# Performance work log

Measured on AMD Instinct MI355X. Metric: run time of the kernel, lower is better.

Reference implementation:

```python
import jax, jax.numpy as jnp
import numpy as np

EPS = 1e-12

def setup_inputs() -> dict:
    key = jax.random.key(0)
    k1, k2 = jax.random.split(key)
    B, C, H, W = 16, 256, 64, 64
    x1 = jax.random.normal(k1, (B, C, H, W), dtype=jnp.float32)
    x2 = jax.random.normal(k2, (B, C, H, W), dtype=jnp.float32)
    return {"x1": x1, "x2": x2}

def _l2norm(x):
    # F.normalize(p=2, dim=2, eps=1e-12): divide by max(norm, eps)
    n = jnp.linalg.norm(x, axis=2, keepdims=True)
    return x / jnp.maximum(n, EPS)

def reference(x1, x2):
    B, C, H, W = x1.shape
    x111 = x1.reshape(B, C, H * W)            # [B,C,N]
    x211 = x2.reshape(B, C, H * W)
    x11 = _l2norm(x111)
    x21 = _l2norm(x211)
    # four CxC score matmuls, fused pairwise adds
    attn1 = jnp.einsum('bcn,bdn->bcd', x11, x11)
    attn2 = jnp.einsum('bcn,bdn->bcd', x21, x21)
    attn0 = jnp.einsum('bcn,bdn->bcd', x21, x11)
    attn00 = jnp.einsum('bcn,bdn->bcd', x11, x21)
    attn11 = jax.nn.softmax(attn1 + attn0, axis=-1)   # [B,C,C]
    attn22 = jax.nn.softmax(attn2 + attn00, axis=-1)
    # back-projection, torch transpose(1,2).reshape(B,C,H,W) semantics
    y1 = jnp.einsum('bcd,bdn->bcn', attn11, x111)     # [B,C,N]
    y2 = jnp.einsum('bcd,bdn->bcn', attn22, x211)
    x1_o = jnp.swapaxes(y1, 1, 2).reshape(B, C, H, W) + x1
    x2_o = jnp.swapaxes(y2, 1, 2).reshape(B, C, H, W) + x2
    return x1_o + x2_o
```

## Files before the change

### kernel.cpp

```cpp
#include <hip/hip_runtime.h>
#include <hip/hip_bf16.h>

#define B_ 16
#define C_ 256
#define N_ 4096
#define CN_ (C_ * N_)

typedef __attribute__((ext_vector_type(8))) short bf16x8_t;
typedef __attribute__((ext_vector_type(4))) float f32x4_t;
typedef unsigned int u32;
typedef unsigned short u16;

__device__ __forceinline__ u16 f2bf(float f) {
    __hip_bfloat16 h = __float2bfloat16(f);
    return __builtin_bit_cast(u16, h);
}
__device__ __forceinline__ float bf2f(u16 u) {
    return __builtin_bit_cast(float, (u32)u << 16);
}

__device__ __forceinline__ void gl_lds16(const void* g, void* l) {
    __builtin_amdgcn_global_load_lds(
        (const __attribute__((address_space(1))) u32*)(g),
        (__attribute__((address_space(3))) u32*)(l), 16, 0, 0);
}

__global__ __launch_bounds__(256) void knorm(const float* __restrict__ x1,
                                             const float* __restrict__ x2,
                                             u16* __restrict__ x1n,
                                             u16* __restrict__ x2n,
                                             u16* __restrict__ sN,
                                             u16* __restrict__ sxb,
                                             float* __restrict__ norms) {
    int row = blockIdx.x;
    int t = threadIdx.x;
    const float4* r1 = (const float4*)(x1 + (size_t)row * N_);
    const float4* r2 = (const float4*)(x2 + (size_t)row * N_);
    float4 a[4], b[4];
    float s1 = 0.f, s2 = 0.f;
#pragma unroll
    for (int p = 0; p < 4; ++p) {
        a[p] = r1[p * 256 + t];
        b[p] = r2[p * 256 + t];
        s1 += a[p].x * a[p].x + a[p].y * a[p].y + a[p].z * a[p].z + a[p].w * a[p].w;
        s2 += b[p].x * b[p].x + b[p].y * b[p].y + b[p].z * b[p].z + b[p].w * b[p].w;
    }
#pragma unroll
    for (int m = 32; m; m >>= 1) { s1 += __shfl_xor(s1, m); s2 += __shfl_xor(s2, m); }
    __shared__ float red[2][4];
    int wid = t >> 6;
    if ((t & 63) == 0) { red[0][wid] = s1; red[1][wid] = s2; }
    __syncthreads();
    s1 = red[0][0] + red[0][1] + red[0][2] + red[0][3];
    s2 = red[1][0] + red[1][1] + red[1][2] + red[1][3];
    float n1 = fmaxf(sqrtf(s1), 1e-12f);
    float n2 = fmaxf(sqrtf(s2), 1e-12f);
    if (t == 0) {
        int bb = row >> 8, cc = row & 255;
        norms[(bb * 2 + 0) * 256 + cc] = n1;
        norms[(bb * 2 + 1) * 256 + cc] = n2;
    }
    float i1 = 1.0f / n1, i2 = 1.0f / n2;
    u16* o1 = x1n + (size_t)row * N_;
    u16* o2 = x2n + (size_t)row * N_;
    u16* os = sN + (size_t)row * N_;
    u16* or_ = sxb + (size_t)row * N_;
#pragma unroll
    for (int p = 0; p < 4; ++p) {
        ushort4 w1, w2, ws, wr;
        w1.x = f2bf(a[p].x * i1); w1.y = f2bf(a[p].y * i1);
        w1.z = f2bf(a[p].z * i1); w1.w = f2bf(a[p].w * i1);
        w2.x = f2bf(b[p].x * i2); w2.y = f2bf(b[p].y * i2);
        w2.z = f2bf(b[p].z * i2); w2.w = f2bf(b[p].w * i2);
        ws.x = f2bf(a[p].x * i1 + b[p].x * i2); ws.y = f2bf(a[p].y * i1 + b[p].y * i2);
        ws.z = f2bf(a[p].z * i1 + b[p].z * i2); ws.w = f2bf(a[p].w * i1 + b[p].w * i2);
        wr.x = f2bf(a[p].x + b[p].x); wr.y = f2bf(a[p].y + b[p].y);
        wr.z = f2bf(a[p].z + b[p].z); wr.w = f2bf(a[p].w + b[p].w);
        size_t off = (size_t)(p * 256 + t) * 4;
        *(ushort4*)(o1 + off) = w1;
        *(ushort4*)(o2 + off) = w2;
        *(ushort4*)(os + off) = ws;
        *(ushort4*)(or_ + off) = wr;
    }
}

__global__ __launch_bounds__(256) void klogits(const u16* __restrict__ sN,
                                               const u16* __restrict__ x1n,
                                               const u16* __restrict__ x2n,
                                               float* __restrict__ logits) {
    int bid = blockIdx.x;
    int xcd = bid & 7;
    int u = bid >> 3;
    int b = xcd + 8 * (u & 1);
    int tile = u >> 1;
    int c0 = (tile & 3) * 64;
    int d0 = (tile >> 2) * 64;

    __shared__ u16 lds[3 * 4096];

    int t = threadIdx.x, lane = t & 63, wid = t >> 6;
    int w = wid & 1, chalf = wid >> 1;

    const char* tb[3];
    tb[0] = (const char*)(sN  + (size_t)b * CN_ + (size_t)c0 * N_);
    tb[1] = (const char*)(x1n + (size_t)b * CN_ + (size_t)d0 * N_);
    tb[2] = (const char*)(x2n + (size_t)b * CN_ + (size_t)d0 * N_);
    const char* gsrc[6];
    char* ldst[6];
#pragma unroll
    for (int qq = 0; qq < 6; ++qq) {
        int q = wid * 6 + qq;
        int ti = q >> 3;
        int s0 = (q & 7) * 1024 + lane * 16;
        int rrow = s0 >> 7, inner = s0 & 127;
        gsrc[qq] = tb[ti] + (size_t)rrow * (N_ * 2) + (inner ^ ((rrow & 7) << 4));
        ldst[qq] = (char*)lds + q * 1024;
    }

    f32x4_t acc[2][4];
#pragma unroll
    for (int i = 0; i < 2; ++i)
#pragma unroll
        for (int j = 0; j < 4; ++j) acc[i][j] = 0.f;

    const char* Abase = (const char*)lds;
    const char* Bbase = (const char*)(lds + (1 + w) * 4096);
    int kl = (lane >> 4) * 16;
    int rA0 = chalf * 32 + (lane & 15);

    for (int ks = 0; ks < 64; ++ks) {
        int kbyte = ks * 128;
#pragma unroll
        for (int qq = 0; qq < 6; ++qq)
            gl_lds16(gsrc[qq] + kbyte, ldst[qq]);
        __syncthreads();
#pragma unroll
        for (int ksub = 0; ksub < 2; ++ksub) {
            int kc = ksub * 64 + kl;
            bf16x8_t af[2], bfr[4];
#pragma unroll
            for (int mi = 0; mi < 2; ++mi) {
                int rr = rA0 + mi * 16;
                af[mi] = *(const bf16x8_t*)(Abase + ((rr << 7) + (kc ^ ((rr & 7) << 4))));
            }
#pragma unroll
            for (int ni = 0; ni < 4; ++ni) {
                int rr = ni * 16 + (lane & 15);
                bfr[ni] = *(const bf16x8_t*)(Bbase + ((rr << 7) + (kc ^ ((rr & 7) << 4))));
            }
#pragma unroll
            for (int mi = 0; mi < 2; ++mi)
#pragma unroll
                for (int ni = 0; ni < 4; ++ni)
                    acc[mi][ni] = __builtin_amdgcn_mfma_f32_16x16x32_bf16(af[mi], bfr[ni], acc[mi][ni], 0, 0, 0);
        }
        __syncthreads();
    }

    float* outp = logits + ((size_t)((b * 2 + w) * 256 + c0 + chalf * 32)) * 256 + d0;
    int orow = (lane >> 4) * 4, ocol = lane & 15;
#pragma unroll
    for (int mi = 0; mi < 2; ++mi)
#pragma unroll
        for (int ni = 0; ni < 4; ++ni)
#pragma unroll
            for (int r = 0; r < 4; ++r)
                outp[(size_t)(mi * 16 + orow + r) * 256 + ni * 16 + ocol] = acc[mi][ni][r];
}

__global__ __launch_bounds__(256) void ksoftmax(const float* __restrict__ logits,
                                                const float* __restrict__ norms,
                                                u16* __restrict__ attnp) {
    int rid = blockIdx.x * 4 + (threadIdx.x >> 6);
    int l = threadIdx.x & 63;
    const float* row = logits + (size_t)rid * 256;
    int bw = rid >> 8;
    float v[4];
    float m = -1e30f;
#pragma unroll
    for (int j = 0; j < 4; ++j) { v[j] = row[j * 64 + l]; m = fmaxf(m, v[j]); }
#pragma unroll
    for (int s = 32; s; s >>= 1) m = fmaxf(m, __shfl_xor(m, s));
    float sum = 0.f;
#pragma unroll
    for (int j = 0; j < 4; ++j) { v[j] = __expf(v[j] - m); sum += v[j]; }
#pragma unroll
    for (int s = 32; s; s >>= 1) sum += __shfl_xor(sum, s);
    float rs = 1.0f / sum;
    u16* outp = attnp + (size_t)rid * 256;
    const float* nr = norms + (size_t)bw * 256;
#pragma unroll
    for (int j = 0; j < 4; ++j)
        outp[j * 64 + l] = f2bf(v[j] * rs * nr[j * 64 + l]);
}

__global__ __launch_bounds__(256) void kout(const u16* __restrict__ x1n,
                                            const u16* __restrict__ x2n,
                                            const u16* __restrict__ attnp,
                                            const u16* __restrict__ sxb,
                                            float* __restrict__ out) {
    int bid = blockIdx.x;
    int xcd = bid & 7;
    int u = bid >> 3;
    int b = xcd + 8 * (u & 1);
    int rest = u >> 1;
    int n0 = (rest >> 1) * 64;
    int c0 = (rest & 1) * 128;

    __shared__ u16 sA[2][4096];
    __shared__ u16 sB[2][8192];

    int t = threadIdx.x, lane = t & 63, wid = t >> 6;
    int wc = wid;

    int tensorA = t >> 7;
    int tt = t & 127;
    int dq = (tt & 15) * 4;
    int n8 = (tt >> 4) * 8;
    const u16* Asrc = (tensorA ? x2n : x1n) + (size_t)b * CN_ + n0 + n8;
    char* sAme = (char*)&sA[tensorA][0];

    const char* gB[8];
    char* lB[8];
#pragma unroll
    for (int qq = 0; qq < 8; ++qq) {
        int q = wid * 8 + qq;
        int tensor = q >> 4;
        int s0 = (q & 15) * 1024 + lane * 16;
        int rrow = s0 >> 7, inner = s0 & 127;
        gB[qq] = (const char*)attnp +
                 ((size_t)((b * 2 + tensor) * 256 + c0 + rrow) * 256) * 2 +
                 (inner ^ ((rrow & 7) << 4));
        lB[qq] = (char*)&sB[0][0] + q * 1024;
    }

    f32x4_t acc1[4][2], acc2[4][2];
#pragma unroll
    for (int i = 0; i < 4; ++i)
#pragma unroll
        for (int j = 0; j < 2; ++j) { acc1[i][j] = 0.f; acc2[i][j] = 0.f; }

    int kl = (lane >> 4) * 16;
    const char* A0 = (const char*)&sA[0][0];
    const char* A1 = (const char*)&sA[1][0];
    const char* B0 = (const char*)&sB[0][0];
    const char* B1 = (const char*)&sB[1][0];

    for (int ks = 0; ks < 4; ++ks) {
        int k0 = ks * 64;
#pragma unroll
        for (int qq = 0; qq < 8; ++qq)
            gl_lds16(gB[qq] + k0 * 2, lB[qq]);
        uint4 r0 = *(const uint4*)(Asrc + (size_t)(k0 + dq + 0) * N_);
        uint4 r1 = *(const uint4*)(Asrc + (size_t)(k0 + dq + 1) * N_);
        uint4 r2 = *(const uint4*)(Asrc + (size_t)(k0 + dq + 2) * N_);
        uint4 r3 = *(const uint4*)(Asrc + (size_t)(k0 + dq + 3) * N_);
        const u16* p0 = (const u16*)&r0;
        const u16* p1 = (const u16*)&r1;
        const u16* p2 = (const u16*)&r2;
        const u16* p3 = (const u16*)&r3;
#pragma unroll
        for (int i = 0; i < 8; ++i) {
            u32 lo = (u32)p0[i] | ((u32)p1[i] << 16);
            u32 hi = (u32)p2[i] | ((u32)p3[i] << 16);
            int n = n8 + i;
            int addr = (n << 7) + (((dq << 1)) ^ ((n & 7) << 4));
            uint2 val; val.x = lo; val.y = hi;
            *(uint2*)(sAme + addr) = val;
        }
        __syncthreads();
#pragma unroll
        for (int ksub = 0; ksub < 2; ++ksub) {
            int kc = ksub * 64 + kl;
            bf16x8_t a1f[4], a2f[4], b1f[2], b2f[2];
#pragma unroll
            for (int mi = 0; mi < 4; ++mi) {
                int rr = mi * 16 + (lane & 15);
                int ao = (rr << 7) + (kc ^ ((rr & 7) << 4));
                a1f[mi] = *(const bf16x8_t*)(A0 + ao);
                a2f[mi] = *(const bf16x8_t*)(A1 + ao);
            }
#pragma unroll
            for (int ci = 0; ci < 2; ++ci) {
                int rr = wc * 32 + ci * 16 + (lane & 15);
                int bo = (rr << 7) + (kc ^ ((rr & 7) << 4));
                b1f[ci] = *(const bf16x8_t*)(B0 + bo);
                b2f[ci] = *(const bf16x8_t*)(B1 + bo);
            }
#pragma unroll
            for (int mi = 0; mi < 4; ++mi)
#pragma unroll
                for (int ci = 0; ci < 2; ++ci) {
                    acc1[mi][ci] = __builtin_amdgcn_mfma_f32_16x16x32_bf16(a1f[mi], b1f[ci], acc1[mi][ci], 0, 0, 0);
                    acc2[mi][ci] = __builtin_amdgcn_mfma_f32_16x16x32_bf16(a2f[mi], b2f[ci], acc2[mi][ci], 0, 0, 0);
                }
        }
        __syncthreads();
    }

    const size_t obase = (size_t)b * CN_;
    int orow = (lane >> 4) * 4, ocol = lane & 15;
#pragma unroll
    for (int mi = 0; mi < 4; ++mi)
#pragma unroll
        for (int ci = 0; ci < 2; ++ci)
#pragma unroll
            for (int r = 0; r < 4; ++r) {
                int n = n0 + mi * 16 + orow + r;
                int c = c0 + wc * 32 + ci * 16 + ocol;
                size_t f = obase + (size_t)n * 256 + c;
                out[f] = acc1[mi][ci][r] + acc2[mi][ci][r] + bf2f(sxb[f]);
            }
}

extern "C" void kernel_launch(void* const* d_in, const int* in_sizes, int n_in,
                              void* d_out, int out_size, void* d_ws, size_t ws_size,
                              hipStream_t stream) {
    const float* x1 = (const float*)d_in[0];
    const float* x2 = (const float*)d_in[1];
    float* out = (float*)d_out;

    char* ws = (char*)d_ws;
    u16*   x1n    = (u16*)(ws);
    u16*   x2n    = (u16*)(ws + 33554432ull);
    u16*   sN     = (u16*)(ws + 67108864ull);
    u16*   sxb    = (u16*)(ws + 100663296ull);
    float* logits = (float*)(ws + 134217728ull);
    u16*   attnp  = (u16*)(ws + 142606336ull);
    float* norms  = (float*)(ws + 146800640ull);

    knorm<<<4096, 256, 0, stream>>>(x1, x2, x1n, x2n, sN, sxb, norms);
    klogits<<<256, 256, 0, stream>>>(sN, x1n, x2n, logits);
    ksoftmax<<<2048, 256, 0, stream>>>(logits, norms, attnp);
    kout<<<2048, 256, 0, stream>>>(x1n, x2n, attnp, sxb, out);
}
```

Before: 272.6 us.

## Split-K logits with double-buffered LDS, restage norm stores, pipeline output GEMM

The logits GEMM is split four ways along N, growing the grid from 256 to 1024 blocks, and its loads are double-buffered in LDS. Partial sums are written to a larger workspace and added together in the softmax kernel. The norm kernel stages rows through LDS so it can issue 16-byte bf16 stores. The output kernel now reads attention fragments straight from global memory instead of through LDS, and prefetches the next A tile into a ping-pong buffer. The aim is better occupancy and latency hiding, at the cost of extra partial-sum traffic and uncached B reads.

```diff
diff --git a/kernel.cpp b/kernel.cpp
--- a/kernel.cpp
+++ b/kernel.cpp
@@ -7,6 +7,7 @@
 #define CN_ (C_ * N_)
 
 typedef __attribute__((ext_vector_type(8))) short bf16x8_t;
+typedef __attribute__((ext_vector_type(8))) unsigned short u16x8_t;
 typedef __attribute__((ext_vector_type(4))) float f32x4_t;
 typedef unsigned int u32;
 typedef unsigned short u16;
@@ -32,18 +33,21 @@
                                              u16* __restrict__ sN,
                                              u16* __restrict__ sxb,
                                              float* __restrict__ norms) {
+    __shared__ float sx1[4096];
+    __shared__ float sx2[4096];
     int row = blockIdx.x;
     int t = threadIdx.x;
     const float4* r1 = (const float4*)(x1 + (size_t)row * N_);
     const float4* r2 = (const float4*)(x2 + (size_t)row * N_);
-    float4 a[4], b[4];
     float s1 = 0.f, s2 = 0.f;
 #pragma unroll
     for (int p = 0; p < 4; ++p) {
-        a[p] = r1[p * 256 + t];
-        b[p] = r2[p * 256 + t];
-        s1 += a[p].x * a[p].x + a[p].y * a[p].y + a[p].z * a[p].z + a[p].w * a[p].w;
-        s2 += b[p].x * b[p].x + b[p].y * b[p].y + b[p].z * b[p].z + b[p].w * b[p].w;
+        float4 a = r1[p * 256 + t];
+        float4 b = r2[p * 256 + t];
+        s1 += a.x * a.x + a.y * a.y + a.z * a.z + a.w * a.w;
+        s2 += b.x * b.x + b.y * b.y + b.z * b.z + b.w * b.w;
+        *(float4*)&sx1[(p * 256 + t) * 4] = a;
+        *(float4*)&sx2[(p * 256 + t) * 4] = b;
     }
 #pragma unroll
     for (int m = 32; m; m >>= 1) { s1 += __shfl_xor(s1, m); s2 += __shfl_xor(s2, m); }
@@ -61,52 +65,55 @@
         norms[(bb * 2 + 1) * 256 + cc] = n2;
     }
     float i1 = 1.0f / n1, i2 = 1.0f / n2;
-    u16* o1 = x1n + (size_t)row * N_;
-    u16* o2 = x2n + (size_t)row * N_;
-    u16* os = sN + (size_t)row * N_;
-    u16* or_ = sxb + (size_t)row * N_;
-#pragma unroll
-    for (int p = 0; p < 4; ++p) {
-        ushort4 w1, w2, ws, wr;
-        w1.x = f2bf(a[p].x * i1); w1.y = f2bf(a[p].y * i1);
-        w1.z = f2bf(a[p].z * i1); w1.w = f2bf(a[p].w * i1);
-        w2.x = f2bf(b[p].x * i2); w2.y = f2bf(b[p].y * i2);
-        w2.z = f2bf(b[p].z * i2); w2.w = f2bf(b[p].w * i2);
-        ws.x = f2bf(a[p].x * i1 + b[p].x * i2); ws.y = f2bf(a[p].y * i1 + b[p].y * i2);
-        ws.z = f2bf(a[p].z * i1 + b[p].z * i2); ws.w = f2bf(a[p].w * i1 + b[p].w * i2);
-        wr.x = f2bf(a[p].x + b[p].x); wr.y = f2bf(a[p].y + b[p].y);
-        wr.z = f2bf(a[p].z + b[p].z); wr.w = f2bf(a[p].w + b[p].w);
-        size_t off = (size_t)(p * 256 + t) * 4;
-        *(ushort4*)(o1 + off) = w1;
-        *(ushort4*)(o2 + off) = w2;
-        *(ushort4*)(os + off) = ws;
-        *(ushort4*)(or_ + off) = wr;
+    const size_t rbase = (size_t)row * N_;
+#pragma unroll
+    for (int j = 0; j < 2; ++j) {
+        int e = j * 2048 + t * 8;
+        float a[8], b[8];
+        *(float4*)&a[0] = *(const float4*)&sx1[e];
+        *(float4*)&a[4] = *(const float4*)&sx1[e + 4];
+        *(float4*)&b[0] = *(const float4*)&sx2[e];
+        *(float4*)&b[4] = *(const float4*)&sx2[e + 4];
+        u16x8_t w1, w2, ws, wr;
+#pragma unroll
+        for (int i = 0; i < 8; ++i) {
+            float va = a[i] * i1, vb = b[i] * i2;
+            w1[i] = f2bf(va);
+            w2[i] = f2bf(vb);
+            ws[i] = f2bf(va + vb);
+            wr[i] = f2bf(a[i] + b[i]);
+        }
+        *(u16x8_t*)(x1n + rbase + e) = w1;
+        *(u16x8_t*)(x2n + rbase + e) = w2;
+        *(u16x8_t*)(sN  + rbase + e) = ws;
+        *(u16x8_t*)(sxb + rbase + e) = wr;
     }
 }
 
 __global__ __launch_bounds__(256) void klogits(const u16* __restrict__ sN,
                                                const u16* __restrict__ x1n,
                                                const u16* __restrict__ x2n,
-                                               float* __restrict__ logits) {
+                                               float* __restrict__ part) {
     int bid = blockIdx.x;
     int xcd = bid & 7;
     int u = bid >> 3;
     int b = xcd + 8 * (u & 1);
-    int tile = u >> 1;
+    int tile = (u >> 1) & 15;
+    int kc4 = u >> 5;
     int c0 = (tile & 3) * 64;
     int d0 = (tile >> 2) * 64;
 
-    __shared__ u16 lds[3 * 4096];
+    __shared__ u16 lds[2][3 * 4096];
 
     int t = threadIdx.x, lane = t & 63, wid = t >> 6;
     int w = wid & 1, chalf = wid >> 1;
 
     const char* tb[3];
-    tb[0] = (const char*)(sN  + (size_t)b * CN_ + (size_t)c0 * N_);
-    tb[1] = (const char*)(x1n + (size_t)b * CN_ + (size_t)d0 * N_);
-    tb[2] = (const char*)(x2n + (size_t)b * CN_ + (size_t)d0 * N_);
+    tb[0] = (const char*)(sN  + (size_t)b * CN_ + (size_t)c0 * N_ + kc4 * 1024);
+    tb[1] = (const char*)(x1n + (size_t)b * CN_ + (size_t)d0 * N_ + kc4 * 1024);
+    tb[2] = (const char*)(x2n + (size_t)b * CN_ + (size_t)d0 * N_ + kc4 * 1024);
     const char* gsrc[6];
-    char* ldst[6];
+    int ldoff[6];
 #pragma unroll
     for (int qq = 0; qq < 6; ++qq) {
         int q = wid * 6 + qq;
@@ -114,7 +121,7 @@
         int s0 = (q & 7) * 1024 + lane * 16;
         int rrow = s0 >> 7, inner = s0 & 127;
         gsrc[qq] = tb[ti] + (size_t)rrow * (N_ * 2) + (inner ^ ((rrow & 7) << 4));
-        ldst[qq] = (char*)lds + q * 1024;
+        ldoff[qq] = q * 1024;
     }
 
     f32x4_t acc[2][4];
@@ -123,17 +130,24 @@
 #pragma unroll
         for (int j = 0; j < 4; ++j) acc[i][j] = 0.f;
 
-    const char* Abase = (const char*)lds;
-    const char* Bbase = (const char*)(lds + (1 + w) * 4096);
     int kl = (lane >> 4) * 16;
     int rA0 = chalf * 32 + (lane & 15);
 
-    for (int ks = 0; ks < 64; ++ks) {
-        int kbyte = ks * 128;
-#pragma unroll
-        for (int qq = 0; qq < 6; ++qq)
-            gl_lds16(gsrc[qq] + kbyte, ldst[qq]);
-        __syncthreads();
+#pragma unroll
+    for (int qq = 0; qq < 6; ++qq)
+        gl_lds16(gsrc[qq], (char*)lds[0] + ldoff[qq]);
+    __syncthreads();
+
+    for (int ks = 0; ks < 16; ++ks) {
+        int p = ks & 1;
+        if (ks < 15) {
+            int kbyte = (ks + 1) * 128;
+#pragma unroll
+            for (int qq = 0; qq < 6; ++qq)
+                gl_lds16(gsrc[qq] + kbyte, (char*)lds[p ^ 1] + ldoff[qq]);
+        }
+        const char* Abase = (const char*)lds[p];
+        const char* Bbase = (const char*)lds[p] + (1 + w) * 8192;
 #pragma unroll
         for (int ksub = 0; ksub < 2; ++ksub) {
             int kc = ksub * 64 + kl;
@@ -157,7 +171,7 @@
         __syncthreads();
     }
 
-    float* outp = logits + ((size_t)((b * 2 + w) * 256 + c0 + chalf * 32)) * 256 + d0;
+    float* outp = part + ((((size_t)kc4 * 16 + b) * 2 + w) * 256 + c0 + chalf * 32) * 256 + d0;
     int orow = (lane >> 4) * 4, ocol = lane & 15;
 #pragma unroll
     for (int mi = 0; mi < 2; ++mi)
@@ -168,17 +182,23 @@
                 outp[(size_t)(mi * 16 + orow + r) * 256 + ni * 16 + ocol] = acc[mi][ni][r];
 }
 
-__global__ __launch_bounds__(256) void ksoftmax(const float* __restrict__ logits,
+__global__ __launch_bounds__(256) void ksoftmax(const float* __restrict__ part,
                                                 const float* __restrict__ norms,
                                                 u16* __restrict__ attnp) {
+    const size_t S = 2097152;
     int rid = blockIdx.x * 4 + (threadIdx.x >> 6);
     int l = threadIdx.x & 63;
-    const float* row = logits + (size_t)rid * 256;
-    int bw = rid >> 8;
+    int bw = rid >> 8, c = rid & 255;
+    size_t rbase = (size_t)bw * 65536 + (size_t)c * 256;
     float v[4];
     float m = -1e30f;
 #pragma unroll
-    for (int j = 0; j < 4; ++j) { v[j] = row[j * 64 + l]; m = fmaxf(m, v[j]); }
+    for (int j = 0; j < 4; ++j) {
+        int d = j * 64 + l;
+        v[j] = part[rbase + d] + part[rbase + S + d] +
+               part[rbase + 2 * S + d] + part[rbase + 3 * S + d];
+        m = fmaxf(m, v[j]);
+    }
 #pragma unroll
     for (int s = 32; s; s >>= 1) m = fmaxf(m, __shfl_xor(m, s));
     float sum = 0.f;
@@ -207,8 +227,7 @@
     int n0 = (rest >> 1) * 64;
     int c0 = (rest & 1) * 128;
 
-    __shared__ u16 sA[2][4096];
-    __shared__ u16 sB[2][8192];
+    __shared__ u16 sA[2][2][4096];
 
     int t = threadIdx.x, lane = t & 63, wid = t >> 6;
     int wc = wid;
@@ -218,21 +237,14 @@
     int dq = (tt & 15) * 4;
     int n8 = (tt >> 4) * 8;
     const u16* Asrc = (tensorA ? x2n : x1n) + (size_t)b * CN_ + n0 + n8;
-    char* sAme = (char*)&sA[tensorA][0];
-
-    const char* gB[8];
-    char* lB[8];
-#pragma unroll
-    for (int qq = 0; qq < 8; ++qq) {
-        int q = wid * 8 + qq;
-        int tensor = q >> 4;
-        int s0 = (q & 15) * 1024 + lane * 16;
-        int rrow = s0 >> 7, inner = s0 & 127;
-        gB[qq] = (const char*)attnp +
-                 ((size_t)((b * 2 + tensor) * 256 + c0 + rrow) * 256) * 2 +
-                 (inner ^ ((rrow & 7) << 4));
-        lB[qq] = (char*)&sB[0][0] + q * 1024;
-    }
+
+    const char* Bb[2][2];
+#pragma unroll
+    for (int tensor = 0; tensor < 2; ++tensor)
+#pragma unroll
+        for (int ci = 0; ci < 2; ++ci)
+            Bb[tensor][ci] = (const char*)(attnp +
+                ((size_t)(b * 2 + tensor) * 256 + c0 + wc * 32 + ci * 16 + (lane & 15)) * 256);
 
     f32x4_t acc1[4][2], acc2[4][2];
 #pragma unroll
@@ -241,37 +253,45 @@
         for (int j = 0; j < 2; ++j) { acc1[i][j] = 0.f; acc2[i][j] = 0.f; }
 
     int kl = (lane >> 4) * 16;
-    const char* A0 = (const char*)&sA[0][0];
-    const char* A1 = (const char*)&sA[1][0];
-    const char* B0 = (const char*)&sB[0][0];
-    const char* B1 = (const char*)&sB[1][0];
+
+    uint4 r0, r1, r2, r3;
+#define LOADA(KS) do { \
+        size_t kk = (size_t)((KS) * 64 + dq); \
+        r0 = *(const uint4*)(Asrc + (kk + 0) * N_); \
+        r1 = *(const uint4*)(Asrc + (kk + 1) * N_); \
+        r2 = *(const uint4*)(Asrc + (kk + 2) * N_); \
+        r3 = *(const uint4*)(Asrc + (kk + 3) * N_); \
+    } while (0)
+#define WRITEA(BUF) do { \
+        const u16* p0 = (const u16*)&r0; \
+        const u16* p1 = (const u16*)&r1; \
+        const u16* p2 = (const u16*)&r2; \
+        const u16* p3 = (const u16*)&r3; \
+        char* dst = (char*)&sA[BUF][tensorA][0]; \
+        _Pragma("unroll") \
+        for (int i = 0; i < 8; ++i) { \
+            u32 lo = (u32)p0[i] | ((u32)p1[i] << 16); \
+            u32 hi = (u32)p2[i] | ((u32)p3[i] << 16); \
+            int n = n8 + i; \
+            int addr = (n << 7) + ((dq << 1) ^ ((n & 7) << 4)); \
+            uint2 val; val.x = lo; val.y = hi; \
+            *(uint2*)(dst + addr) = val; \
+        } \
+    } while (0)
+
+    LOADA(0);
+    WRITEA(0);
 
     for (int ks = 0; ks < 4; ++ks) {
-        int k0 = ks * 64;
-#pragma unroll
-        for (int qq = 0; qq < 8; ++qq)
-            gl_lds16(gB[qq] + k0 * 2, lB[qq]);
-        uint4 r0 = *(const uint4*)(Asrc + (size_t)(k0 + dq + 0) * N_);
-        uint4 r1 = *(const uint4*)(Asrc + (size_t)(k0 + dq + 1) * N_);
-        uint4 r2 = *(const uint4*)(Asrc + (size_t)(k0 + dq + 2) * N_);
-        uint4 r3 = *(const uint4*)(Asrc + (size_t)(k0 + dq + 3) * N_);
-        const u16* p0 = (const u16*)&r0;
-        const u16* p1 = (const u16*)&r1;
-        const u16* p2 = (const u16*)&r2;
-        const u16* p3 = (const u16*)&r3;
-#pragma unroll
-        for (int i = 0; i < 8; ++i) {
-            u32 lo = (u32)p0[i] | ((u32)p1[i] << 16);
-            u32 hi = (u32)p2[i] | ((u32)p3[i] << 16);
-            int n = n8 + i;
-            int addr = (n << 7) + (((dq << 1)) ^ ((n & 7) << 4));
-            uint2 val; val.x = lo; val.y = hi;
-            *(uint2*)(sAme + addr) = val;
-        }
+        int p = ks & 1;
         __syncthreads();
+        if (ks < 3) LOADA(ks + 1);
+        const char* A0 = (const char*)&sA[p][0][0];
+        const char* A1 = (const char*)&sA[p][1][0];
 #pragma unroll
         for (int ksub = 0; ksub < 2; ++ksub) {
             int kc = ksub * 64 + kl;
+            int kb = ks * 128 + kc;
             bf16x8_t a1f[4], a2f[4], b1f[2], b2f[2];
 #pragma unroll
             for (int mi = 0; mi < 4; ++mi) {
@@ -282,10 +302,8 @@
             }
 #pragma unroll
             for (int ci = 0; ci < 2; ++ci) {
-                int rr = wc * 32 + ci * 16 + (lane & 15);
-                int bo = (rr << 7) + (kc ^ ((rr & 7) << 4));
-                b1f[ci] = *(const bf16x8_t*)(B0 + bo);
-                b2f[ci] = *(const bf16x8_t*)(B1 + bo);
+                b1f[ci] = *(const bf16x8_t*)(Bb[0][ci] + kb);
+                b2f[ci] = *(const bf16x8_t*)(Bb[1][ci] + kb);
             }
 #pragma unroll
             for (int mi = 0; mi < 4; ++mi)
@@ -295,7 +313,7 @@
                     acc2[mi][ci] = __builtin_amdgcn_mfma_f32_16x16x32_bf16(a2f[mi], b2f[ci], acc2[mi][ci], 0, 0, 0);
                 }
         }
-        __syncthreads();
+        if (ks < 3) WRITEA(p ^ 1);
     }
 
     const size_t obase = (size_t)b * CN_;
@@ -311,6 +329,8 @@
                 size_t f = obase + (size_t)n * 256 + c;
                 out[f] = acc1[mi][ci][r] + acc2[mi][ci][r] + bf2f(sxb[f]);
             }
+#undef LOADA
+#undef WRITEA
 }
 
 extern "C" void kernel_launch(void* const* d_in, const int* in_sizes, int n_in,
@@ -321,16 +341,16 @@
     float* out = (float*)d_out;
 
     char* ws = (char*)d_ws;
-    u16*   x1n    = (u16*)(ws);
-    u16*   x2n    = (u16*)(ws + 33554432ull);
-    u16*   sN     = (u16*)(ws + 67108864ull);
-    u16*   sxb    = (u16*)(ws + 100663296ull);
-    float* logits = (float*)(ws + 134217728ull);
-    u16*   attnp  = (u16*)(ws + 142606336ull);
-    float* norms  = (float*)(ws + 146800640ull);
+    u16*   x1n   = (u16*)(ws);
+    u16*   x2n   = (u16*)(ws + 33554432ull);
+    u16*   sN    = (u16*)(ws + 67108864ull);
+    u16*   sxb   = (u16*)(ws + 100663296ull);
+    float* part  = (float*)(ws + 134217728ull);
+    u16*   attnp = (u16*)(ws + 167772160ull);
+    float* norms = (float*)(ws + 171966464ull);
 
     knorm<<<4096, 256, 0, stream>>>(x1, x2, x1n, x2n, sN, sxb, norms);
-    klogits<<<256, 256, 0, stream>>>(sN, x1n, x2n, logits);
-    ksoftmax<<<2048, 256, 0, stream>>>(logits, norms, attnp);
+    klogits<<<1024, 256, 0, stream>>>(sN, x1n, x2n, part);
+    ksoftmax<<<2048, 256, 0, stream>>>(part, norms, attnp);
     kout<<<2048, 256, 0, stream>>>(x1n, x2n, attnp, sxb, out);
 }
```

After: 274.3 us. About the same (+0.6%).
